# Performance work log

Measured on AMD Instinct MI355X. Metric: run time of the kernel, lower is better.

## Reference

```python
import jax, jax.numpy as jnp
import numpy as np

B, L, D_IN, D_OUT = 4, 256, 256, 256


def setup_inputs() -> dict:
    key = jax.random.key(0)
    k1, k2, k3, k4, k5 = jax.random.split(key, 5)
    text = jax.random.normal(k1, (B, L, D_IN), dtype=jnp.float32)
    adj = jax.random.uniform(k2, (B, L, L), dtype=jnp.float32)
    dep_embed = jax.random.normal(k3, (B, L, L, D_IN), dtype=jnp.float32)
    # nn.Linear default init scale ~ 1/sqrt(fan_in); use small random weights
    W = jax.random.normal(k4, (D_OUT, D_IN), dtype=jnp.float32) / jnp.sqrt(D_IN).astype(jnp.float32)
    b = jax.random.normal(k5, (D_OUT,), dtype=jnp.float32) * 0.01
    return {"text": text, "adj": adj, "dep_embed": dep_embed, "W": W, "b": b}


def reference(text, adj, dep_embed, W, b):
    # val_sum[b,i,j,d] = text[b,i,d] + dep_embed[b,i,j,d]   -> [B,L,L,D]
    val_sum = text[:, :, None, :] + dep_embed
    # hidden = Linear(val_sum): [B,L,L,D_out]
    hidden = jnp.einsum('bijd,od->bijo', val_sum, W) + b
    # output[b,i,o] = sum_j hidden[b,j,i,o] * adj[b,i,j]  (transpose(1,2) then adj-mask then sum over dim 2)
    output = jnp.einsum('bjio,bij->bio', hidden, adj)
    return output
```

## Files before the change

### kernel.cpp

```cpp
#include <hip/hip_runtime.h>


#define LL 256
#define DD 256
#define D4 64

__global__ __launch_bounds__(256) void tgc_fused_kernel(
    const float* __restrict__ text,
    const float* __restrict__ adj,
    const float* __restrict__ dep,
    const float* __restrict__ W,
    const float* __restrict__ bias,
    float* __restrict__ out)
{
    const int bi = blockIdx.x;
    const int b  = bi >> 8;
    const int i  = bi & 255;
    const int t  = threadIdx.x;
    const int g  = t >> 6;
    const int l  = t & 63;

    __shared__ float  adjs[LL];
    __shared__ float4 red[4][64];
    __shared__ float  ared[4];
    __shared__ float4 sfin[64];

    adjs[t] = adj[bi * LL + t];
    __syncthreads();

    const float4* text4 = (const float4*)text;
    const float4* dep4  = (const float4*)dep;

    float4 acc = make_float4(0.f, 0.f, 0.f, 0.f);
    float  asum = 0.f;

    #pragma unroll 8
    for (int jj = 0; jj < 64; ++jj) {
        const int j = (jj << 2) + g;
        const float a  = adjs[j];
        const float4 tv = text4[(b * LL + j) * D4 + l];
        const float4 dv = dep4[((b * LL + j) * LL + i) * D4 + l];
        acc.x += a * (tv.x + dv.x);
        acc.y += a * (tv.y + dv.y);
        acc.z += a * (tv.z + dv.z);
        acc.w += a * (tv.w + dv.w);
        asum  += a;
    }

    red[g][l] = acc;
    if (l == 0) ared[g] = asum;
    __syncthreads();

    if (g == 0) {
        const float4 r0 = red[0][l], r1 = red[1][l], r2 = red[2][l], r3 = red[3][l];
        float4 s;
        s.x = r0.x + r1.x + r2.x + r3.x;
        s.y = r0.y + r1.y + r2.y + r3.y;
        s.z = r0.z + r1.z + r2.z + r3.z;
        s.w = r0.w + r1.w + r2.w + r3.w;
        sfin[l] = s;
    }
    __syncthreads();

    const float A = ared[0] + ared[1] + ared[2] + ared[3];

    const float4* W4 = (const float4*)W;
    float oacc = 0.f;
    #pragma unroll 8
    for (int d4 = 0; d4 < D4; ++d4) {
        const float4 s = sfin[d4];
        const float4 w = W4[t * D4 + d4];
        oacc += s.x * w.x + s.y * w.y + s.z * w.z + s.w * w.w;
    }
    out[bi * DD + t] = oacc + A * bias[t];
}

extern "C" void kernel_launch(void* const* d_in, const int* in_sizes, int n_in,
                              void* d_out, int out_size, void* d_ws, size_t ws_size,
                              hipStream_t stream) {
    const float* text = (const float*)d_in[0];
    const float* adj  = (const float*)d_in[1];
    const float* dep  = (const float*)d_in[2];
    const float* W    = (const float*)d_in[3];
    const float* bias = (const float*)d_in[4];
    float* out = (float*)d_out;

    tgc_fused_kernel<<<dim3(1024), dim3(256), 0, stream>>>(text, adj, dep, W, bias, out);
}
```

Baseline: 384.0 us.

## Split fused kernel into j-partitioned reduction and projection phases

Splits the kernel into two launches. The first covers a tile of 8 consecutive i rows and 32 j values, so each dep access is a contiguous 8 KB span and each text row is reused across the 8 rows. It writes per-j-group partial sums to workspace. The second kernel sums the 8 partials, computes the adj row sum with wavefront shuffles, and applies W and bias. This targets the strided, poorly coalesced dep access of the original loop, at the cost of an extra launch and a round trip through the workspace.

Measured after the change: 401.3 us. +4.5%, slower.

```diff
diff --git a/kernel.cpp b/kernel.cpp
--- a/kernel.cpp
+++ b/kernel.cpp
@@ -1,14 +1,74 @@
 #include <hip/hip_runtime.h>
 
 
-#define LL 256
-#define DD 256
-#define D4 64
+#define LL  256
+#define DD  256
+#define D4  64
+#define G   8
+#define JPG 32
+#define ICL 8
 
-__global__ __launch_bounds__(256) void tgc_fused_kernel(
+__global__ __launch_bounds__(256) void tgc_phase1(
     const float* __restrict__ text,
     const float* __restrict__ adj,
     const float* __restrict__ dep,
+    float* __restrict__ sp)
+{
+    const int bid = blockIdx.x;
+    const int ic  = bid & 31;
+    const int jg  = (bid >> 5) & (G - 1);
+    const int b   = bid >> 8;
+    const int i0  = ic * ICL;
+    const int j0  = jg * JPG;
+    const int t   = threadIdx.x;
+    const int w   = t >> 6;
+    const int l   = t & 63;
+
+    __shared__ float adjs[ICL][JPG];
+
+    {
+        const int k  = t >> 5;
+        const int jl = t & 31;
+        adjs[k][jl] = adj[((b * LL) + i0 + k) * LL + j0 + jl];
+    }
+    __syncthreads();
+
+    const float4* __restrict__ dep4  = (const float4*)dep;
+    const float4* __restrict__ text4 = (const float4*)text;
+
+    float4 acc0 = make_float4(0.f, 0.f, 0.f, 0.f);
+    float4 acc1 = make_float4(0.f, 0.f, 0.f, 0.f);
+
+    const float4* dp = dep4 + ((size_t)(b * LL + j0) * LL + i0) * D4;
+    const float4* tp = text4 + ((size_t)(b * LL + j0) * D4 + l);
+    const size_t  JS = (size_t)LL * D4;
+
+    #pragma unroll 4
+    for (int jl = 0; jl < JPG; ++jl) {
+        const float  a0 = adjs[w][jl];
+        const float  a1 = adjs[4 + w][jl];
+        const float4 tv = tp[(size_t)jl * D4];
+        const float4 d0 = dp[(size_t)jl * JS + t];
+        const float4 d1 = dp[(size_t)jl * JS + t + 256];
+        acc0.x += a0 * (tv.x + d0.x);
+        acc0.y += a0 * (tv.y + d0.y);
+        acc0.z += a0 * (tv.z + d0.z);
+        acc0.w += a0 * (tv.w + d0.w);
+        acc1.x += a1 * (tv.x + d1.x);
+        acc1.y += a1 * (tv.y + d1.y);
+        acc1.z += a1 * (tv.z + d1.z);
+        acc1.w += a1 * (tv.w + d1.w);
+    }
+
+    float4* sp4 = (float4*)sp;
+    const size_t base = ((size_t)(b * G + jg) * LL + i0) * D4;
+    sp4[base + (size_t)(w)     * D4 + l] = acc0;
+    sp4[base + (size_t)(4 + w) * D4 + l] = acc1;
+}
+
+__global__ __launch_bounds__(256) void tgc_phase2(
+    const float* __restrict__ adj,
+    const float* __restrict__ sp,
     const float* __restrict__ W,
     const float* __restrict__ bias,
     float* __restrict__ out)
@@ -17,48 +77,30 @@
     const int b  = bi >> 8;
     const int i  = bi & 255;
     const int t  = threadIdx.x;
-    const int g  = t >> 6;
+    const int w  = t >> 6;
     const int l  = t & 63;
 
-    __shared__ float  adjs[LL];
     __shared__ float4 red[4][64];
     __shared__ float  ared[4];
     __shared__ float4 sfin[64];
 
-    adjs[t] = adj[bi * LL + t];
+    float av = adj[bi * LL + t];
+    #pragma unroll
+    for (int off = 32; off > 0; off >>= 1) av += __shfl_down(av, off);
+    if (l == 0) ared[w] = av;
+
+    const float4* sp4 = (const float4*)sp;
+    const float4  s0 = sp4[((size_t)(b * G + w)     * LL + i) * D4 + l];
+    const float4  s1 = sp4[((size_t)(b * G + 4 + w) * LL + i) * D4 + l];
+    red[w][l] = make_float4(s0.x + s1.x, s0.y + s1.y, s0.z + s1.z, s0.w + s1.w);
     __syncthreads();
 
-    const float4* text4 = (const float4*)text;
-    const float4* dep4  = (const float4*)dep;
-
-    float4 acc = make_float4(0.f, 0.f, 0.f, 0.f);
-    float  asum = 0.f;
-
-    #pragma unroll 8
-    for (int jj = 0; jj < 64; ++jj) {
-        const int j = (jj << 2) + g;
-        const float a  = adjs[j];
-        const float4 tv = text4[(b * LL + j) * D4 + l];
-        const float4 dv = dep4[((b * LL + j) * LL + i) * D4 + l];
-        acc.x += a * (tv.x + dv.x);
-        acc.y += a * (tv.y + dv.y);
-        acc.z += a * (tv.z + dv.z);
-        acc.w += a * (tv.w + dv.w);
-        asum  += a;
-    }
-
-    red[g][l] = acc;
-    if (l == 0) ared[g] = asum;
-    __syncthreads();
-
-    if (g == 0) {
+    if (w == 0) {
         const float4 r0 = red[0][l], r1 = red[1][l], r2 = red[2][l], r3 = red[3][l];
-        float4 s;
-        s.x = r0.x + r1.x + r2.x + r3.x;
-        s.y = r0.y + r1.y + r2.y + r3.y;
-        s.z = r0.z + r1.z + r2.z + r3.z;
-        s.w = r0.w + r1.w + r2.w + r3.w;
-        sfin[l] = s;
+        sfin[l] = make_float4(r0.x + r1.x + r2.x + r3.x,
+                              r0.y + r1.y + r2.y + r3.y,
+                              r0.z + r1.z + r2.z + r3.z,
+                              r0.w + r1.w + r2.w + r3.w);
     }
     __syncthreads();
 
@@ -68,9 +110,9 @@
     float oacc = 0.f;
     #pragma unroll 8
     for (int d4 = 0; d4 < D4; ++d4) {
-        const float4 s = sfin[d4];
-        const float4 w = W4[t * D4 + d4];
-        oacc += s.x * w.x + s.y * w.y + s.z * w.z + s.w * w.w;
+        const float4 s  = sfin[d4];
+        const float4 wv = W4[t * D4 + d4];
+        oacc += s.x * wv.x + s.y * wv.y + s.z * wv.z + s.w * wv.w;
     }
     out[bi * DD + t] = oacc + A * bias[t];
 }
@@ -84,6 +126,8 @@
     const float* W    = (const float*)d_in[3];
     const float* bias = (const float*)d_in[4];
     float* out = (float*)d_out;
+    float* sp  = (float*)d_ws;
 
-    tgc_fused_kernel<<<dim3(1024), dim3(256), 0, stream>>>(text, adj, dep, W, bias, out);
+    tgc_phase1<<<dim3(4 * G * 32), dim3(256), 0, stream>>>(text, adj, dep, sp);
+    tgc_phase2<<<dim3(4 * LL), dim3(256), 0, stream>>>(adj, sp, W, bias, out);
 }
```

## Split fused kernel into j-split reduction phase and projection phase

Applied to the files above, without the earlier changes.

The single fused kernel is split in two. The first kernel uses 2048 blocks, each reducing half of the j range over dep_embed with nontemporal loads, with the text term in a separate loop, and writes partial sums to workspace. The second kernel combines the two partials, sums adj with wave shuffles, and applies the W projection. The goal is more blocks in flight and better streaming of the 256MB dep tensor, at the cost of an extra launch and a workspace round trip.

New measurement: 377.2 us. Within noise of the previous version (-1.8%).

```diff
diff --git a/kernel.cpp b/kernel.cpp
--- a/kernel.cpp
+++ b/kernel.cpp
@@ -5,60 +5,98 @@
 #define DD 256
 #define D4 64
 
-__global__ __launch_bounds__(256) void tgc_fused_kernel(
+typedef float float4n __attribute__((ext_vector_type(4)));
+
+__global__ __launch_bounds__(256, 8) void tgc_phase1(
     const float* __restrict__ text,
     const float* __restrict__ adj,
     const float* __restrict__ dep,
+    float4* __restrict__ spS)
+{
+    const int bid = blockIdx.x;
+    const int jh  = bid & 1;
+    const int bi  = bid >> 1;
+    const int b   = bi >> 8;
+    const int i   = bi & 255;
+    const int t   = threadIdx.x;
+    const int g   = t >> 6;
+    const int l   = t & 63;
+
+    __shared__ float  adjs[128];
+    __shared__ float4 red[4][64];
+
+    if (t < 128) adjs[t] = adj[bi * LL + jh * 128 + t];
+    __syncthreads();
+
+    const float4n* __restrict__ dep4 = (const float4n*)dep;
+    const float4*  __restrict__ text4 = (const float4*)text;
+
+    float4 acc = make_float4(0.f, 0.f, 0.f, 0.f);
+
+    {
+        const float4n* dp = dep4 + (((size_t)(b * LL + jh * 128 + g) * LL + i) * D4 + l);
+        const size_t   JS = (size_t)4 * LL * D4;
+        #pragma unroll 4
+        for (int jj = 0; jj < 32; ++jj) {
+            const float   a = adjs[(jj << 2) + g];
+            const float4n d = __builtin_nontemporal_load(dp);
+            acc.x += a * d.x;
+            acc.y += a * d.y;
+            acc.z += a * d.z;
+            acc.w += a * d.w;
+            dp += JS;
+        }
+    }
+    {
+        const float4* tp = text4 + ((size_t)(b * LL + jh * 128 + g) * D4 + l);
+        const size_t  TS = (size_t)4 * D4;
+        #pragma unroll 4
+        for (int jj = 0; jj < 32; ++jj) {
+            const float  a  = adjs[(jj << 2) + g];
+            const float4 tv = *tp;
+            acc.x += a * tv.x;
+            acc.y += a * tv.y;
+            acc.z += a * tv.z;
+            acc.w += a * tv.w;
+            tp += TS;
+        }
+    }
+
+    red[g][l] = acc;
+    __syncthreads();
+    if (g == 0) {
+        const float4 r0 = red[0][l], r1 = red[1][l], r2 = red[2][l], r3 = red[3][l];
+        spS[(size_t)bid * 64 + l] = make_float4(r0.x + r1.x + r2.x + r3.x,
+                                                r0.y + r1.y + r2.y + r3.y,
+                                                r0.z + r1.z + r2.z + r3.z,
+                                                r0.w + r1.w + r2.w + r3.w);
+    }
+}
+
+__global__ __launch_bounds__(256) void tgc_phase2(
+    const float* __restrict__ adj,
+    const float4* __restrict__ spS,
     const float* __restrict__ W,
     const float* __restrict__ bias,
     float* __restrict__ out)
 {
     const int bi = blockIdx.x;
-    const int b  = bi >> 8;
-    const int i  = bi & 255;
     const int t  = threadIdx.x;
-    const int g  = t >> 6;
+    const int w  = t >> 6;
     const int l  = t & 63;
 
-    __shared__ float  adjs[LL];
-    __shared__ float4 red[4][64];
+    __shared__ float4 sfin[64];
     __shared__ float  ared[4];
-    __shared__ float4 sfin[64];
 
-    adjs[t] = adj[bi * LL + t];
-    __syncthreads();
+    float av = adj[bi * LL + t];
+    #pragma unroll
+    for (int off = 32; off > 0; off >>= 1) av += __shfl_down(av, off);
+    if (l == 0) ared[w] = av;
 
-    const float4* text4 = (const float4*)text;
-    const float4* dep4  = (const float4*)dep;
-
-    float4 acc = make_float4(0.f, 0.f, 0.f, 0.f);
-    float  asum = 0.f;
-
-    #pragma unroll 8
-    for (int jj = 0; jj < 64; ++jj) {
-        const int j = (jj << 2) + g;
-        const float a  = adjs[j];
-        const float4 tv = text4[(b * LL + j) * D4 + l];
-        const float4 dv = dep4[((b * LL + j) * LL + i) * D4 + l];
-        acc.x += a * (tv.x + dv.x);
-        acc.y += a * (tv.y + dv.y);
-        acc.z += a * (tv.z + dv.z);
-        acc.w += a * (tv.w + dv.w);
-        asum  += a;
-    }
-
-    red[g][l] = acc;
-    if (l == 0) ared[g] = asum;
-    __syncthreads();
-
-    if (g == 0) {
-        const float4 r0 = red[0][l], r1 = red[1][l], r2 = red[2][l], r3 = red[3][l];
-        float4 s;
-        s.x = r0.x + r1.x + r2.x + r3.x;
-        s.y = r0.y + r1.y + r2.y + r3.y;
-        s.z = r0.z + r1.z + r2.z + r3.z;
-        s.w = r0.w + r1.w + r2.w + r3.w;
-        sfin[l] = s;
+    if (w == 0) {
+        const float4 s0 = spS[(size_t)(bi * 2)     * 64 + l];
+        const float4 s1 = spS[(size_t)(bi * 2 + 1) * 64 + l];
+        sfin[l] = make_float4(s0.x + s1.x, s0.y + s1.y, s0.z + s1.z, s0.w + s1.w);
     }
     __syncthreads();
 
@@ -68,9 +106,9 @@
     float oacc = 0.f;
     #pragma unroll 8
     for (int d4 = 0; d4 < D4; ++d4) {
-        const float4 s = sfin[d4];
-        const float4 w = W4[t * D4 + d4];
-        oacc += s.x * w.x + s.y * w.y + s.z * w.z + s.w * w.w;
+        const float4 s  = sfin[d4];
+        const float4 wv = W4[t * D4 + d4];
+        oacc += s.x * wv.x + s.y * wv.y + s.z * wv.z + s.w * wv.w;
     }
     out[bi * DD + t] = oacc + A * bias[t];
 }
@@ -84,6 +122,8 @@
     const float* W    = (const float*)d_in[3];
     const float* bias = (const float*)d_in[4];
     float* out = (float*)d_out;
+    float4* spS = (float4*)d_ws;
 
-    tgc_fused_kernel<<<dim3(1024), dim3(256), 0, stream>>>(text, adj, dep, W, bias, out);
+    tgc_phase1<<<dim3(2048), dim3(256), 0, stream>>>(text, adj, dep, spS);
+    tgc_phase2<<<dim3(1024), dim3(256), 0, stream>>>(adj, spS, W, bias, out);
 }
```
